# Optimization experiments

Measured on AMD Instinct MI355X. Metric: run time of the kernel, lower is better.

The kernel has to match this reference:

```python
import jax, jax.numpy as jnp
import numpy as np

B, N, C = 8, 2048, 256
EPS = 1e-6


def _l2_norm(x):
    return x / (jnp.linalg.norm(x, axis=-1, keepdims=True) + EPS)


def setup_inputs() -> dict:
    key = jax.random.key(0)
    ks = jax.random.split(key, 13)
    s = 1.0 / np.sqrt(C)
    def lin(k):
        kw, kb = jax.random.split(k)
        return (jax.random.normal(kw, (C, C), jnp.float32) * s,
                jax.random.normal(kb, (C,), jnp.float32) * 0.01)
    Wq, bq = lin(ks[0]); Wk, bk = lin(ks[1]); Wv, bv = lin(ks[2])
    Wa, ba = lin(ks[3]); Wb, bb = lin(ks[4]); Wo, bo = lin(ks[5])
    x = jax.random.normal(ks[6], (B, N, C), jnp.float32)
    return {"x": x, "Wq": Wq, "bq": bq, "Wk": Wk, "bk": bk, "Wv": Wv, "bv": bv,
            "Wa": Wa, "ba": ba, "Wb": Wb, "bb": bb, "Wo": Wo, "bo": bo}


def reference(x, Wq, bq, Wk, bk, Wv, bv, Wa, ba, Wb, bb, Wo, bo):
    Bs, Ns, Cs = x.shape
    # projections (torch Linear: y = x @ W.T + b)
    q = _l2_norm(jax.nn.silu(x @ Wq.T + bq))          # [B,N,C]
    k = _l2_norm(jax.nn.silu(x @ Wk.T + bk))
    v = jax.nn.silu(x @ Wv.T + bv)
    a = jax.nn.sigmoid(x @ Wa.T + ba).mean(-1)       # [B,N] per-step scalar gate
    b = jax.nn.sigmoid(x @ Wb.T + bb).mean(-1)       # [B,N]

    eye = jnp.eye(Cs, dtype=x.dtype)

    def step(S, inp):
        qt, kt, vt, at, bt = inp                      # [B,C],[B,C],[B,C],[B],[B]
        kkT = kt[:, :, None] * kt[:, None, :]         # [B,C,C]
        decay = eye[None] - bt[:, None, None] * kkT
        S = at[:, None, None] * jnp.matmul(S, decay) \
            + bt[:, None, None] * (vt[:, :, None] * kt[:, None, :])
        # ot_j = sum_i q_i * S_ji  ==  S @ q
        ot = jnp.einsum('bij,bj->bi', S, qt)
        return S, ot

    S0 = jnp.zeros((Bs, Cs, Cs), dtype=x.dtype)
    xs = (jnp.swapaxes(q, 0, 1), jnp.swapaxes(k, 0, 1), jnp.swapaxes(v, 0, 1),
          a.T, b.T)                                   # time-major [N, ...]
    _, O = jax.lax.scan(step, S0, xs)                 # O: [N,B,C]
    O = jnp.swapaxes(O, 0, 1)                         # [B,N,C]
    return O @ Wo.T + bo
```

## Files before the change

### kernel.cpp

```cpp
#include <hip/hip_runtime.h>
#include <math.h>

#define B_ 8
#define N_ 2048
#define C_ 256
#define TOK (B_*N_)
#define T_ 64
#define NCH (N_/T_)

typedef __bf16 bf16x8 __attribute__((ext_vector_type(8)));
typedef float f32x4v __attribute__((ext_vector_type(4)));

__device__ __forceinline__ float dot4(const float4& a, const float4& b) {
  return (a.x*b.x + a.y*b.y) + (a.z*b.z + a.w*b.w);
}
__device__ __forceinline__ float rdlane(float x, int idx) {
  return __int_as_float(__builtin_amdgcn_readlane(__float_as_int(x), idx));
}
__device__ __forceinline__ float bf2f(unsigned short u) {
  return __uint_as_float(((unsigned)u) << 16);
}
__device__ __forceinline__ unsigned short f2bf(float f) {
  unsigned x = __float_as_uint(f);
  return (unsigned short)((x + 0x7FFFu + ((x >> 16) & 1u)) >> 16);
}

__global__ __launch_bounds__(256) void split_pack(const float* __restrict__ src,
                                                  unsigned short* __restrict__ hi,
                                                  unsigned short* __restrict__ lo) {
  const size_t f = ((size_t)blockIdx.x * 256 + threadIdx.x) * 4;
  float4 v = *(const float4*)(src + f);
  const int row = (int)(f >> 8);
  const int k   = (int)(f & 255);
  const int R = row >> 4, lr = row & 15;
  const int ks = k >> 5, kg = (k >> 3) & 3, ki = k & 7;
  const size_t pos = ((((size_t)R*8 + ks)*64) + kg*16 + lr)*8 + ki;
  ushort4 H, L;
  H.x = f2bf(v.x); H.y = f2bf(v.y); H.z = f2bf(v.z); H.w = f2bf(v.w);
  L.x = f2bf(v.x - bf2f(H.x));
  L.y = f2bf(v.y - bf2f(H.y));
  L.z = f2bf(v.z - bf2f(H.z));
  L.w = f2bf(v.w - bf2f(H.w));
  *(ushort4*)(hi + pos) = H;
  *(ushort4*)(lo + pos) = L;
}

template<int EPI>
__global__ __launch_bounds__(256) void proj_v3(const unsigned short* __restrict__ xh,
                                               const unsigned short* __restrict__ xl,
                                               const unsigned short* __restrict__ wh,
                                               const unsigned short* __restrict__ wl,
                                               const float* __restrict__ bias,
                                               float* __restrict__ out) {
  __shared__ float redp[4][20];
  const int tid = threadIdx.x;
  const int l = tid & 63, w = tid >> 6;
  const int lc = l & 15, kg = l >> 4;
  const int rb = blockIdx.x * 16;
  const size_t Rbase = (size_t)blockIdx.x * 8;

  f32x4v acc[4];
  #pragma unroll
  for (int nt2 = 0; nt2 < 4; ++nt2) acc[nt2] = (f32x4v){0.f, 0.f, 0.f, 0.f};

  #pragma unroll
  for (int ks = 0; ks < 8; ++ks) {
    const size_t apos = ((Rbase + ks)*64 + l)*8;
    bf16x8 ah = *reinterpret_cast<const bf16x8*>(xh + apos);
    bf16x8 al = *reinterpret_cast<const bf16x8*>(xl + apos);
    #pragma unroll
    for (int nt2 = 0; nt2 < 4; ++nt2) {
      const size_t bpos = (((size_t)(w*4 + nt2)*8 + ks)*64 + l)*8;
      bf16x8 bh = *reinterpret_cast<const bf16x8*>(wh + bpos);
      bf16x8 bl = *reinterpret_cast<const bf16x8*>(wl + bpos);
      acc[nt2] = __builtin_amdgcn_mfma_f32_16x16x32_bf16(ah, bh, acc[nt2], 0, 0, 0);
      acc[nt2] = __builtin_amdgcn_mfma_f32_16x16x32_bf16(ah, bl, acc[nt2], 0, 0, 0);
      acc[nt2] = __builtin_amdgcn_mfma_f32_16x16x32_bf16(al, bh, acc[nt2], 0, 0, 0);
    }
  }

  const int row0 = kg * 4;

  if constexpr (EPI == 3) {
    #pragma unroll
    for (int nt2 = 0; nt2 < 4; ++nt2) {
      const float bval = bias[w*64 + nt2*16 + lc];
      #pragma unroll
      for (int e = 0; e < 4; ++e)
        out[(size_t)(rb + row0 + e)*C_ + w*64 + nt2*16 + lc] = acc[nt2][e] + bval;
    }
  } else if constexpr (EPI == 1) {
    #pragma unroll
    for (int nt2 = 0; nt2 < 4; ++nt2) {
      const float bval = bias[w*64 + nt2*16 + lc];
      #pragma unroll
      for (int e = 0; e < 4; ++e) {
        float y = acc[nt2][e] + bval;
        out[(size_t)(rb + row0 + e)*C_ + w*64 + nt2*16 + lc] = y / (1.f + __expf(-y));
      }
    }
  } else if constexpr (EPI == 0) {
    float part[4] = {0.f, 0.f, 0.f, 0.f};
    #pragma unroll
    for (int nt2 = 0; nt2 < 4; ++nt2) {
      const float bval = bias[w*64 + nt2*16 + lc];
      #pragma unroll
      for (int e = 0; e < 4; ++e) {
        float y = acc[nt2][e] + bval;
        float s = y / (1.f + __expf(-y));
        acc[nt2][e] = s;
        part[e] += s * s;
      }
    }
    #pragma unroll
    for (int e = 0; e < 4; ++e) {
      float r = part[e];
      r += __shfl_xor(r, 1, 64);
      r += __shfl_xor(r, 2, 64);
      r += __shfl_xor(r, 4, 64);
      r += __shfl_xor(r, 8, 64);
      part[e] = r;
    }
    if (lc == 0) {
      #pragma unroll
      for (int e = 0; e < 4; ++e) redp[w][row0 + e] = part[e];
    }
    __syncthreads();
    #pragma unroll
    for (int e = 0; e < 4; ++e) {
      float s = redp[0][row0+e] + redp[1][row0+e] + redp[2][row0+e] + redp[3][row0+e];
      part[e] = 1.f / (sqrtf(s) + 1e-6f);
    }
    #pragma unroll
    for (int nt2 = 0; nt2 < 4; ++nt2)
      #pragma unroll
      for (int e = 0; e < 4; ++e)
        out[(size_t)(rb + row0 + e)*C_ + w*64 + nt2*16 + lc] = acc[nt2][e] * part[e];
  } else {
    float part[4] = {0.f, 0.f, 0.f, 0.f};
    #pragma unroll
    for (int nt2 = 0; nt2 < 4; ++nt2) {
      const float bval = bias[w*64 + nt2*16 + lc];
      #pragma unroll
      for (int e = 0; e < 4; ++e) {
        float y = acc[nt2][e] + bval;
        part[e] += 1.f / (1.f + __expf(-y));
      }
    }
    #pragma unroll
    for (int e = 0; e < 4; ++e) {
      float r = part[e];
      r += __shfl_xor(r, 1, 64);
      r += __shfl_xor(r, 2, 64);
      r += __shfl_xor(r, 4, 64);
      r += __shfl_xor(r, 8, 64);
      part[e] = r;
    }
    if (lc == 0) {
      #pragma unroll
      for (int e = 0; e < 4; ++e) redp[w][row0 + e] = part[e];
    }
    __syncthreads();
    if (w == 0 && lc == 0) {
      #pragma unroll
      for (int e = 0; e < 4; ++e) {
        float s = redp[0][row0+e] + redp[1][row0+e] + redp[2][row0+e] + redp[3][row0+e];
        out[rb + row0 + e] = s * (1.f / 256.f);
      }
    }
  }
}

__global__ __launch_bounds__(256) void chunk_prep(const float* __restrict__ kn,
                                                  const float* __restrict__ qn,
                                                  float* __restrict__ vO,
                                                  const float* __restrict__ Ag,
                                                  const float* __restrict__ Bg,
                                                  float* __restrict__ Ubuf,
                                                  float* __restrict__ qrm,
                                                  float* __restrict__ gbuf,
                                                  float* __restrict__ Oout) {
  __shared__ float Gl[64][68];
  __shared__ float Wl[64][68];
  __shared__ float pool[17408];
  __shared__ float gam[64], al[64], bl[64];
  float* Kp = pool;
  float* Qp = pool + 4096;
  const int bid = blockIdx.x;
  const int b = bid & 7, c = bid >> 3;
  const size_t ct0 = (size_t)b*N_ + (size_t)c*T_;
  const size_t base = ct0 * C_;
  const int tid = threadIdx.x;
  const int lane = tid & 63;
  const int sg = tid >> 6;

  if (tid < 64) { al[tid] = Ag[ct0 + tid]; bl[tid] = Bg[ct0 + tid]; }

  float accG[16], accQ[16];
  #pragma unroll
  for (int m = 0; m < 16; ++m) { accG[m] = 0.f; accQ[m] = 0.f; }
  for (int p = 0; p < 4; ++p) {
    __syncthreads();
    #pragma unroll
    for (int i = 0; i < 4; ++i) {
      int idx = i*256 + tid;
      int t = idx >> 4, u = idx & 15;
      int phys = (t*16 + (u ^ (t & 15))) * 4;
      *(float4*)&Kp[phys] = *(const float4*)(kn + base + (size_t)t*C_ + p*64 + u*4);
      *(float4*)&Qp[phys] = *(const float4*)(qn + base + (size_t)t*C_ + p*64 + u*4);
    }
    __syncthreads();
    #pragma unroll 4
    for (int j4 = 0; j4 < 16; ++j4) {
      float4 kt = *(const float4*)&Kp[(lane*16 + (j4 ^ (lane & 15))) * 4];
      float4 qt = *(const float4*)&Qp[(lane*16 + (j4 ^ (lane & 15))) * 4];
      #pragma unroll
      for (int m = 0; m < 16; ++m) {
        int r = sg*16 + m;
        float4 ks = *(const float4*)&Kp[(r*16 + (j4 ^ (r & 15))) * 4];
        accG[m] += dot4(kt, ks);
        accQ[m] += dot4(qt, ks);
      }
    }
  }
  __syncthreads();
  #pragma unroll
  for (int m = 0; m < 16; ++m) {
    int col = sg*16 + m;
    Gl[lane][col] = (col <  lane) ? accG[m] : 0.f;
    Wl[lane][col] = (col <= lane) ? accQ[m] : 0.f;
  }
  __syncthreads();
  if (tid == 0) {
    float g = 1.f;
    for (int s = 0; s < 64; ++s) { g *= al[s]; gam[s] = g; }
  }
  __syncthreads();
  if (tid < 64) gbuf[ct0 + tid] = gam[tid];
  __syncthreads();

  const int j = tid;
  float* const myrow = &pool[j * 68];

  for (int s = 0; s < 64; ++s) {
    float a0 = kn[base + (size_t)s*C_ + j], a1 = 0.f, a2 = 0.f, a3 = 0.f;
    for (int r4 = 0; r4 <= (s >> 2); ++r4) {
      float4 g = *(const float4*)&Gl[s][r4*4];
      float4 uu = *(const float4*)&myrow[r4*4];
      a0 -= g.x*uu.x; a1 -= g.y*uu.y; a2 -= g.z*uu.z; a3 -= g.w*uu.w;
    }
    float us = bl[s] * ((a0 + a1) + (a2 + a3));
    myrow[s] = us;
    Ubuf[base + (size_t)s*C_ + j] = us;
  }

  for (int t = 0; t < 64; ++t) {
    float a0 = qn[base + (size_t)t*C_ + j], a1 = 0.f, a2 = 0.f, a3 = 0.f;
    for (int s4 = 0; s4 < 16; ++s4) {
      float4 w = *(const float4*)&Wl[t][s4*4];
      float4 uu = *(const float4*)&myrow[s4*4];
      a0 -= w.x*uu.x; a1 -= w.y*uu.y; a2 -= w.z*uu.z; a3 -= w.w*uu.w;
    }
    qrm[base + (size_t)t*C_ + j] = (a0 + a1) + (a2 + a3);
  }

  __syncthreads();
  #pragma unroll
  for (int p2 = 0; p2 < 16; ++p2) {
    int idx = p2*256 + tid; int s = idx >> 6, r = idx & 63;
    float rs = gam[s] / gam[r];
    Gl[s][r] *= rs;
    Wl[s][r] *= rs;
  }
  __syncthreads();
  const float gT = gam[63];

  for (int s = 0; s < 64; ++s) {
    float a0 = vO[base + (size_t)s*C_ + j], a1 = 0.f, a2 = 0.f, a3 = 0.f;
    for (int r4 = 0; r4 <= (s >> 2); ++r4) {
      float4 g = *(const float4*)&Gl[s][r4*4];
      float4 yy = *(const float4*)&myrow[r4*4];
      a0 -= g.x*yy.x; a1 -= g.y*yy.y; a2 -= g.z*yy.z; a3 -= g.w*yy.w;
    }
    myrow[s] = bl[s] * ((a0 + a1) + (a2 + a3));
  }
  __syncthreads();
  for (int s4 = 0; s4 < 16; ++s4) {
    float4 yy = *(const float4*)&myrow[s4*4];
    float z0 = (gT / gam[s4*4+0]) * yy.x;
    float z1 = (gT / gam[s4*4+1]) * yy.y;
    float z2 = (gT / gam[s4*4+2]) * yy.z;
    float z3 = (gT / gam[s4*4+3]) * yy.w;
    *(float4*)&vO[base + (size_t)j*64 + s4*4] = make_float4(z0, z1, z2, z3);
  }
  for (int t = 0; t < 64; ++t) {
    float a0 = 0.f, a1 = 0.f, a2 = 0.f, a3 = 0.f;
    for (int s4 = 0; s4 < 16; ++s4) {
      float4 w = *(const float4*)&Wl[t][s4*4];
      float4 yy = *(const float4*)&myrow[s4*4];
      a0 += w.x*yy.x; a1 += w.y*yy.y; a2 += w.z*yy.z; a3 += w.w*yy.w;
    }
    Oout[base + (size_t)t*C_ + j] = (a0 + a1) + (a2 + a3);
  }
}

__global__ __launch_bounds__(256) void chunk_scan(const float* __restrict__ kn,
                                                  const float* __restrict__ qrm,
                                                  const float* __restrict__ urm,
                                                  const float* __restrict__ ztT,
                                                  const float* __restrict__ gbuf,
                                                  float* __restrict__ Oout) {
  __shared__ float Qs[16384];
  __shared__ float Us[16384];
  __shared__ float red[4*64*20];
  const int bid = blockIdx.x;
  const int b = bid & 7;
  const int wgrp = bid >> 3;
  const int tid = threadIdx.x;
  const int wave = tid >> 6, lane = tid & 63;
  const int i0 = wgrp*8;
  const int lx = lane & 15;

  float S_[8];
  #pragma unroll
  for (int r = 0; r < 8; ++r) S_[r] = 0.f;

  for (int ch = 0; ch < NCH; ++ch) {
    const size_t ct0 = (size_t)b*N_ + (size_t)ch*T_;
    const size_t base = ct0 * C_;

    #pragma unroll
    for (int i = 0; i < 16; ++i) {
      int g = i*256 + tid;
      int t = g >> 6, u = g & 63;
      int phys = (t*64 + (u ^ (t & 15))) * 4;
      *(float4*)&Qs[phys] = *(const float4*)(qrm + base + (size_t)g*4);
      *(float4*)&Us[phys] = *(const float4*)(urm + base + (size_t)g*4);
    }
    __syncthreads();

    const float gv = gbuf[ct0 + lane];
    const float gT = rdlane(gv, 63);

    float oA[8], dB[8];
    #pragma unroll
    for (int r = 0; r < 8; ++r) { oA[r] = 0.f; dB[r] = 0.f; }
    #pragma unroll
    for (int uu = 0; uu < 16; ++uu) {
      const int u = (wave << 4) + uu;
      float4 qv = *(const float4*)&Qs[(lane*64 + (u ^ lx)) * 4];
      float4 uv = *(const float4*)&Us[(lane*64 + (u ^ lx)) * 4];
      #pragma unroll
      for (int m = 0; m < 4; ++m) {
        const int jl = 4*uu + m;
        const float qm = (m==0) ? qv.x : (m==1) ? qv.y : (m==2) ? qv.z : qv.w;
        const float um = (m==0) ? uv.x : (m==1) ? uv.y : (m==2) ? uv.z : uv.w;
        #pragma unroll
        for (int r = 0; r < 8; ++r) {
          const float sv = rdlane(S_[r], jl);
          oA[r] += sv * qm;
          dB[r] += sv * um;
        }
      }
    }
    {
      float* rp = &red[(wave*64 + lane) * 20];
      *(float4*)&rp[0]  = make_float4(oA[0], oA[1], oA[2], oA[3]);
      *(float4*)&rp[4]  = make_float4(oA[4], oA[5], oA[6], oA[7]);
      *(float4*)&rp[8]  = make_float4(dB[0], dB[1], dB[2], dB[3]);
      *(float4*)&rp[12] = make_float4(dB[4], dB[5], dB[6], dB[7]);
    }
    __syncthreads();

    #pragma unroll
    for (int i = 0; i < 16; ++i) {
      int idx = (i*256 + tid) * 4;
      *(float4*)&Qs[idx] = *(const float4*)(kn + base + idx);
    }

    #pragma unroll
    for (int r = 0; r < 8; ++r) { oA[r] = 0.f; dB[r] = 0.f; }
    #pragma unroll
    for (int w2 = 0; w2 < 4; ++w2) {
      const float* rp = &red[(w2*64 + lane) * 20];
      float4 a = *(const float4*)&rp[0];
      float4 bq = *(const float4*)&rp[4];
      float4 cq = *(const float4*)&rp[8];
      float4 dq = *(const float4*)&rp[12];
      oA[0] += a.x;  oA[1] += a.y;  oA[2] += a.z;  oA[3] += a.w;
      oA[4] += bq.x; oA[5] += bq.y; oA[6] += bq.z; oA[7] += bq.w;
      dB[0] += cq.x; dB[1] += cq.y; dB[2] += cq.z; dB[3] += cq.w;
      dB[4] += dq.x; dB[5] += dq.y; dB[6] += dq.z; dB[7] += dq.w;
    }
    #pragma unroll
    for (int r = 0; r < 8; ++r) {
      const float z = ztT[base + (size_t)(i0 + r)*64 + lane];
      dB[r] = gT*dB[r] - z;
    }
    if (wave == 0) {
      float* orow = Oout + base + (size_t)lane*C_ + i0;
      float4 o0 = *(float4*)&orow[0];
      float4 o1 = *(float4*)&orow[4];
      o0.x += gv*oA[0]; o0.y += gv*oA[1]; o0.z += gv*oA[2]; o0.w += gv*oA[3];
      o1.x += gv*oA[4]; o1.y += gv*oA[5]; o1.z += gv*oA[6]; o1.w += gv*oA[7];
      *(float4*)&orow[0] = o0;
      *(float4*)&orow[4] = o1;
    }
    __syncthreads();

    float acc[8];
    #pragma unroll
    for (int r = 0; r < 8; ++r) acc[r] = 0.f;
    const int jcol = (wave << 6) + lane;
    #pragma unroll 8
    for (int s = 0; s < 64; ++s) {
      const float kv = Qs[s*256 + jcol];
      #pragma unroll
      for (int r = 0; r < 8; ++r)
        acc[r] += rdlane(dB[r], s) * kv;
    }
    #pragma unroll
    for (int r = 0; r < 8; ++r) S_[r] = gT*S_[r] - acc[r];
    __syncthreads();
  }
}

extern "C" void kernel_launch(void* const* d_in, const int* in_sizes, int n_in,
                              void* d_out, int out_size, void* d_ws, size_t ws_size,
                              hipStream_t stream) {
  const float* x  = (const float*)d_in[0];
  const float* Wq = (const float*)d_in[1];  const float* bq = (const float*)d_in[2];
  const float* Wk = (const float*)d_in[3];  const float* bk = (const float*)d_in[4];
  const float* Wv = (const float*)d_in[5];  const float* bv = (const float*)d_in[6];
  const float* Wa = (const float*)d_in[7];  const float* ba = (const float*)d_in[8];
  const float* Wb = (const float*)d_in[9];  const float* bb = (const float*)d_in[10];
  const float* Wo = (const float*)d_in[11]; const float* bo = (const float*)d_in[12];

  float* ws = (float*)d_ws;
  const size_t TC = (size_t)TOK * C_;
  float* qn   = ws;
  float* kn   = ws + TC;
  float* vO   = ws + 2*TC;
  float* Ag   = ws + 3*TC;
  float* Bg   = Ag + TOK;
  float* gbuf = Bg + TOK;
  float* Ubuf = gbuf + TOK;
  float* qrm  = Ubuf + TC;

  unsigned short* xhi = (unsigned short*)Ubuf;
  unsigned short* xlo = xhi + TC;
  unsigned short* whd = (unsigned short*)d_out;
  unsigned short* whiU = (unsigned short*)Ubuf;
  unsigned short* wloU = whiU + 65536;
  unsigned short* ohi = (unsigned short*)qrm;
  unsigned short* olo = ohi + TC;

  split_pack<<<dim3(TC/1024), 256, 0, stream>>>(x, xhi, xlo);
  split_pack<<<dim3(64), 256, 0, stream>>>(Wq, whd + 0*131072, whd + 0*131072 + 65536);
  split_pack<<<dim3(64), 256, 0, stream>>>(Wk, whd + 1*131072, whd + 1*131072 + 65536);
  split_pack<<<dim3(64), 256, 0, stream>>>(Wv, whd + 2*131072, whd + 2*131072 + 65536);
  split_pack<<<dim3(64), 256, 0, stream>>>(Wa, whd + 3*131072, whd + 3*131072 + 65536);
  split_pack<<<dim3(64), 256, 0, stream>>>(Wb, whd + 4*131072, whd + 4*131072 + 65536);
  proj_v3<0><<<dim3(TOK/16), 256, 0, stream>>>(xhi, xlo, whd + 0*131072, whd + 0*131072 + 65536, bq, qn);
  proj_v3<0><<<dim3(TOK/16), 256, 0, stream>>>(xhi, xlo, whd + 1*131072, whd + 1*131072 + 65536, bk, kn);
  proj_v3<1><<<dim3(TOK/16), 256, 0, stream>>>(xhi, xlo, whd + 2*131072, whd + 2*131072 + 65536, bv, vO);
  proj_v3<2><<<dim3(TOK/16), 256, 0, stream>>>(xhi, xlo, whd + 3*131072, whd + 3*131072 + 65536, ba, Ag);
  proj_v3<2><<<dim3(TOK/16), 256, 0, stream>>>(xhi, xlo, whd + 4*131072, whd + 4*131072 + 65536, bb, Bg);
  chunk_prep<<<dim3(256), 256, 0, stream>>>(kn, qn, vO, Ag, Bg, Ubuf, qrm, gbuf,
                                            (float*)d_out);
  chunk_scan<<<dim3(256), 256, 0, stream>>>(kn, qrm, Ubuf, vO, gbuf,
                                            (float*)d_out);
  split_pack<<<dim3(64), 256, 0, stream>>>(Wo, whiU, wloU);
  split_pack<<<dim3(TC/1024), 256, 0, stream>>>((const float*)d_out, ohi, olo);
  proj_v3<3><<<dim3(TOK/16), 256, 0, stream>>>(ohi, olo, whiU, wloU, bo,
                                               (float*)d_out);
}
```

Baseline: 588.9 us.

## Split chunk_scan state rows across two wave groups with 512-thread blocks

Doubles chunk_scan workgroup size to 512 threads and splits each block's 8 state rows into two halves of 4, one per group of 4 waves. Each wave now keeps 4 state rows instead of 8, which halves the readlane/FMA work per wave in the sequential chunk loop and gives more waves per CU to hide latency. The reduction buffer layout and the global-to-LDS load loops are adjusted to match. In exchange, the K and Q/U tiles are loaded once per block but consumed by twice as many waves, and the barriers now synchronise a larger workgroup.

Result: faster. 568.2 us (-3.5%).

```diff
diff --git a/kernel.cpp b/kernel.cpp
--- a/kernel.cpp
+++ b/kernel.cpp
@@ -304,7 +304,7 @@
   }
 }
 
-__global__ __launch_bounds__(256) void chunk_scan(const float* __restrict__ kn,
+__global__ __launch_bounds__(512) void chunk_scan(const float* __restrict__ kn,
                                                   const float* __restrict__ qrm,
                                                   const float* __restrict__ urm,
                                                   const float* __restrict__ ztT,
@@ -312,26 +312,27 @@
                                                   float* __restrict__ Oout) {
   __shared__ float Qs[16384];
   __shared__ float Us[16384];
-  __shared__ float red[4*64*20];
+  __shared__ float red[8*64*12];
   const int bid = blockIdx.x;
   const int b = bid & 7;
   const int wgrp = bid >> 3;
   const int tid = threadIdx.x;
   const int wave = tid >> 6, lane = tid & 63;
-  const int i0 = wgrp*8;
+  const int half = wave >> 2, jq = wave & 3;
+  const int i0h = wgrp*8 + half*4;
   const int lx = lane & 15;
 
-  float S_[8];
-  #pragma unroll
-  for (int r = 0; r < 8; ++r) S_[r] = 0.f;
+  float S_[4];
+  #pragma unroll
+  for (int r = 0; r < 4; ++r) S_[r] = 0.f;
 
   for (int ch = 0; ch < NCH; ++ch) {
     const size_t ct0 = (size_t)b*N_ + (size_t)ch*T_;
     const size_t base = ct0 * C_;
 
     #pragma unroll
-    for (int i = 0; i < 16; ++i) {
-      int g = i*256 + tid;
+    for (int i = 0; i < 8; ++i) {
+      int g = i*512 + tid;
       int t = g >> 6, u = g & 63;
       int phys = (t*64 + (u ^ (t & 15))) * 4;
       *(float4*)&Qs[phys] = *(const float4*)(qrm + base + (size_t)g*4);
@@ -342,12 +343,12 @@
     const float gv = gbuf[ct0 + lane];
     const float gT = rdlane(gv, 63);
 
-    float oA[8], dB[8];
-    #pragma unroll
-    for (int r = 0; r < 8; ++r) { oA[r] = 0.f; dB[r] = 0.f; }
+    float oA[4], dB[4];
+    #pragma unroll
+    for (int r = 0; r < 4; ++r) { oA[r] = 0.f; dB[r] = 0.f; }
     #pragma unroll
     for (int uu = 0; uu < 16; ++uu) {
-      const int u = (wave << 4) + uu;
+      const int u = (jq << 4) + uu;
       float4 qv = *(const float4*)&Qs[(lane*64 + (u ^ lx)) * 4];
       float4 uv = *(const float4*)&Us[(lane*64 + (u ^ lx)) * 4];
       #pragma unroll
@@ -356,7 +357,7 @@
         const float qm = (m==0) ? qv.x : (m==1) ? qv.y : (m==2) ? qv.z : qv.w;
         const float um = (m==0) ? uv.x : (m==1) ? uv.y : (m==2) ? uv.z : uv.w;
         #pragma unroll
-        for (int r = 0; r < 8; ++r) {
+        for (int r = 0; r < 4; ++r) {
           const float sv = rdlane(S_[r], jl);
           oA[r] += sv * qm;
           dB[r] += sv * um;
@@ -364,63 +365,54 @@
       }
     }
     {
-      float* rp = &red[(wave*64 + lane) * 20];
-      *(float4*)&rp[0]  = make_float4(oA[0], oA[1], oA[2], oA[3]);
-      *(float4*)&rp[4]  = make_float4(oA[4], oA[5], oA[6], oA[7]);
-      *(float4*)&rp[8]  = make_float4(dB[0], dB[1], dB[2], dB[3]);
-      *(float4*)&rp[12] = make_float4(dB[4], dB[5], dB[6], dB[7]);
-    }
-    __syncthreads();
-
-    #pragma unroll
-    for (int i = 0; i < 16; ++i) {
-      int idx = (i*256 + tid) * 4;
+      float* rp = &red[(wave*64 + lane) * 12];
+      *(float4*)&rp[0] = make_float4(oA[0], oA[1], oA[2], oA[3]);
+      *(float4*)&rp[4] = make_float4(dB[0], dB[1], dB[2], dB[3]);
+    }
+    __syncthreads();
+
+    #pragma unroll
+    for (int i = 0; i < 8; ++i) {
+      int idx = (i*512 + tid) * 4;
       *(float4*)&Qs[idx] = *(const float4*)(kn + base + idx);
     }
 
     #pragma unroll
-    for (int r = 0; r < 8; ++r) { oA[r] = 0.f; dB[r] = 0.f; }
-    #pragma unroll
-    for (int w2 = 0; w2 < 4; ++w2) {
-      const float* rp = &red[(w2*64 + lane) * 20];
+    for (int r = 0; r < 4; ++r) { oA[r] = 0.f; dB[r] = 0.f; }
+    #pragma unroll
+    for (int jq2 = 0; jq2 < 4; ++jq2) {
+      const float* rp = &red[((half*4 + jq2)*64 + lane) * 12];
       float4 a = *(const float4*)&rp[0];
-      float4 bq = *(const float4*)&rp[4];
-      float4 cq = *(const float4*)&rp[8];
-      float4 dq = *(const float4*)&rp[12];
-      oA[0] += a.x;  oA[1] += a.y;  oA[2] += a.z;  oA[3] += a.w;
-      oA[4] += bq.x; oA[5] += bq.y; oA[6] += bq.z; oA[7] += bq.w;
-      dB[0] += cq.x; dB[1] += cq.y; dB[2] += cq.z; dB[3] += cq.w;
-      dB[4] += dq.x; dB[5] += dq.y; dB[6] += dq.z; dB[7] += dq.w;
-    }
-    #pragma unroll
-    for (int r = 0; r < 8; ++r) {
-      const float z = ztT[base + (size_t)(i0 + r)*64 + lane];
+      float4 d = *(const float4*)&rp[4];
+      oA[0] += a.x; oA[1] += a.y; oA[2] += a.z; oA[3] += a.w;
+      dB[0] += d.x; dB[1] += d.y; dB[2] += d.z; dB[3] += d.w;
+    }
+    #pragma unroll
+    for (int r = 0; r < 4; ++r) {
+      const float z = ztT[base + (size_t)(i0h + r)*64 + lane];
       dB[r] = gT*dB[r] - z;
     }
-    if (wave == 0) {
-      float* orow = Oout + base + (size_t)lane*C_ + i0;
+    if (jq == 0) {
+      float* orow = Oout + base + (size_t)lane*C_ + i0h;
       float4 o0 = *(float4*)&orow[0];
-      float4 o1 = *(float4*)&orow[4];
       o0.x += gv*oA[0]; o0.y += gv*oA[1]; o0.z += gv*oA[2]; o0.w += gv*oA[3];
-      o1.x += gv*oA[4]; o1.y += gv*oA[5]; o1.z += gv*oA[6]; o1.w += gv*oA[7];
       *(float4*)&orow[0] = o0;
-      *(float4*)&orow[4] = o1;
-    }
-    __syncthreads();
-
-    float acc[8];
-    #pragma unroll
-    for (int r = 0; r < 8; ++r) acc[r] = 0.f;
-    const int jcol = (wave << 6) + lane;
+    }
+    __syncthreads();
+
+    float acc[4];
+    #pragma unroll
+    for (int r = 0; r < 4; ++r) acc[r] = 0.f;
+    const int jcol = (jq << 6) + lane;
     #pragma unroll 8
     for (int s = 0; s < 64; ++s) {
       const float kv = Qs[s*256 + jcol];
       #pragma unroll
-      for (int r = 0; r < 8; ++r)
+      for (int r = 0; r < 4; ++r)
         acc[r] += rdlane(dB[r], s) * kv;
     }
     #pragma unroll
-    for (int r = 0; r < 8; ++r) S_[r] = gT*S_[r] - acc[r];
+    for (int r = 0; r < 4; ++r) S_[r] = gT*S_[r] - acc[r];
     __syncthreads();
   }
 }
@@ -468,7 +460,7 @@
   proj_v3<2><<<dim3(TOK/16), 256, 0, stream>>>(xhi, xlo, whd + 4*131072, whd + 4*131072 + 65536, bb, Bg);
   chunk_prep<<<dim3(256), 256, 0, stream>>>(kn, qn, vO, Ag, Bg, Ubuf, qrm, gbuf,
                                             (float*)d_out);
-  chunk_scan<<<dim3(256), 256, 0, stream>>>(kn, qrm, Ubuf, vO, gbuf,
+  chunk_scan<<<dim3(256), 512, 0, stream>>>(kn, qrm, Ubuf, vO, gbuf,
                                             (float*)d_out);
   split_pack<<<dim3(64), 256, 0, stream>>>(Wo, whiU, wloU);
   split_pack<<<dim3(TC/1024), 256, 0, stream>>>((const float*)d_out, ohi, olo);
```
